# Kernel optimization log

Hardware: AMD Instinct MI355X
Metric: run time of the kernel (lower is better)

## Reference

```python
import jax, jax.numpy as jnp
import numpy as np

B, T, C = 8, 2048, 1024
DK = 64  # d_k = n_embd // n_head = 1024 // 16


def setup_inputs() -> dict:
    key = jax.random.key(0)
    ks = jax.random.split(key, 4)
    X = jax.random.normal(ks[0], (B, T, C), dtype=jnp.float32)
    scale = 1.0 / np.sqrt(C)
    Wq = jax.random.normal(ks[1], (C, DK), dtype=jnp.float32) * scale
    Wk = jax.random.normal(ks[2], (C, DK), dtype=jnp.float32) * scale
    Wv = jax.random.normal(ks[3], (C, DK), dtype=jnp.float32) * scale
    bq = jnp.zeros((DK,), dtype=jnp.float32)
    bk = jnp.zeros((DK,), dtype=jnp.float32)
    bv = jnp.zeros((DK,), dtype=jnp.float32)
    return {"X": X, "Wq": Wq, "bq": bq, "Wk": Wk, "bk": bk, "Wv": Wv, "bv": bv}


def reference(X, Wq, bq, Wk, bk, Wv, bv):
    # Single-head causal self-attention (dropout disabled / eval mode).
    T_ = X.shape[1]
    Q = X @ Wq + bq  # [B, T, d_k]
    K = X @ Wk + bk
    V = X @ Wv + bv
    scores = jnp.einsum('btd,bsd->bts', Q, K) / jnp.sqrt(jnp.float32(Q.shape[-1]))
    causal = jnp.tril(jnp.ones((T_, T_), dtype=bool))  # tril mask
    scores = jnp.where(causal, scores, -jnp.inf)
    weights = jax.nn.softmax(scores, axis=-1)
    out = jnp.einsum('bts,bsd->btd', weights, V)  # [B, T, d_k]
    return out
```

## Files before the change

### kernel.cpp

```cpp
#include <hip/hip_runtime.h>
#include <math.h>

#define NB 8
#define NT 2048
#define NC 1024
#define DK 64
#define BT (NB*NT)

#define QKV_BYTES  (3u * BT * DK * 2u)
#define SLOT_BYTES 8704u

typedef unsigned short ushort_t;
typedef unsigned int uint_t;
typedef __attribute__((ext_vector_type(8))) short short8;
typedef __attribute__((ext_vector_type(4))) float f32x4;

__device__ __forceinline__ float bf2f(uint_t u) {
    union { uint_t i; float f; } v;
    v.i = u << 16;
    return v.f;
}
__device__ __forceinline__ ushort_t f2bf(float f) {
    union { float f; uint_t i; } v; v.f = f;
    uint_t x = v.i;
    return (ushort_t)((x + 0x7fffu + ((x >> 16) & 1u)) >> 16);
}
__device__ __forceinline__ uint_t pack2bf(float lo, float hi) {
    return (uint_t)f2bf(lo) | ((uint_t)f2bf(hi) << 16);
}

__device__ __forceinline__ int seg_prefix(int qt) {
    const int a = qt >> 2;
    return 2 * a * (a + 1) - 4 + (qt & 3) * (a + 1);
}

__global__ __launch_bounds__(256) void wt_prep_kernel(
    const float* __restrict__ Wq, const float* __restrict__ Wk,
    const float* __restrict__ Wv, ushort_t* __restrict__ WtP)
{
    const int tid = blockIdx.x * 256 + threadIdx.x;
    int idx = tid;
    const int lane = idx & 63;  idx >>= 6;
    const int j    = idx % 6;   idx /= 6;
    const int w    = idx & 3;   idx >>= 2;
    const int ks   = idx & 7;   idx >>= 3;
    const int grp  = idx & 1;

    const int col = lane & 15;
    const int g   = lane >> 4;
    const int tj  = j >> 1;
    const int c   = j & 1;
    const int ng  = 48 * w + 16 * tj + col;
    const int which = ng >> 6, ncol = ng & 63;
    const float* W = (which == 0) ? Wq : (which == 1) ? Wk : Wv;
    const int kb = grp * 512 + ks * 64 + 32 * c + 8 * g;

    ushort_t o[8];
    #pragma unroll
    for (int i = 0; i < 8; ++i) o[i] = f2bf(W[(size_t)(kb + i) * DK + ncol]);
    *reinterpret_cast<uint4*>(&WtP[(size_t)tid * 8]) = *reinterpret_cast<uint4*>(o);
}

__global__ __launch_bounds__(512, 4) void qkv_mfma_kernel(
    const float* __restrict__ X, const ushort_t* __restrict__ WtP,
    const float* __restrict__ bq, const float* __restrict__ bk,
    const float* __restrict__ bv, ushort_t* __restrict__ QKV)
{
    __shared__ ushort_t Xs[2][2][32 * 72];
    __shared__ float    Racc[32 * 196];
    __shared__ ushort_t VtL[64 * 40];

    const int t    = threadIdx.x;
    const int grp  = t >> 8;
    const int tg   = t & 255;
    const int w    = (t >> 6) & 3;
    const int lane = t & 63;
    const int g    = lane >> 4;
    const int col  = lane & 15;
    const int m0   = blockIdx.x * 32;
    const int kb   = grp * 512;

    const int xrow = tg >> 3;
    const int xc   = (tg & 7) * 8;

    float xfA[8], xfB[8];
    short8 wA[6], wB[6];

    auto LOADX = [&](int k0, float* xf) {
        const float4* xp = reinterpret_cast<const float4*>(
            &X[(size_t)(m0 + xrow) * NC + kb + k0 + xc]);
        float4 v0 = xp[0], v1 = xp[1];
        xf[0] = v0.x; xf[1] = v0.y; xf[2] = v0.z; xf[3] = v0.w;
        xf[4] = v1.x; xf[5] = v1.y; xf[6] = v1.z; xf[7] = v1.w;
    };
    auto LOADW = [&](int ks, short8* wn) {
        const ushort_t* base = WtP + ((size_t)((grp * 8 + ks) * 4 + w)) * (6 * 64 * 8);
        #pragma unroll
        for (int j = 0; j < 6; ++j)
            wn[j] = *reinterpret_cast<const short8*>(base + (j * 64 + lane) * 8);
    };
    auto WRITEX = [&](int b, const float* xf) {
        ushort_t xb[8];
        #pragma unroll
        for (int j = 0; j < 8; ++j) xb[j] = f2bf(xf[j]);
        *reinterpret_cast<uint4*>(&Xs[grp][b][xrow * 72 + xc]) =
            *reinterpret_cast<uint4*>(xb);
    };

    f32x4 acc[2][3];
    #pragma unroll
    for (int ri = 0; ri < 2; ++ri)
        #pragma unroll
        for (int tj = 0; tj < 3; ++tj) acc[ri][tj] = (f32x4){0.f, 0.f, 0.f, 0.f};

    auto COMPUTE = [&](int cur, short8* wc) {
        const ushort_t* XsB = Xs[grp][cur];
        #pragma unroll
        for (int c = 0; c < 2; ++c) {
            short8 af[2];
            #pragma unroll
            for (int ri = 0; ri < 2; ++ri)
                af[ri] = *reinterpret_cast<const short8*>(
                    &XsB[(16 * ri + col) * 72 + 32 * c + 8 * g]);
            #pragma unroll
            for (int ri = 0; ri < 2; ++ri)
                #pragma unroll
                for (int tj = 0; tj < 3; ++tj)
                    acc[ri][tj] = __builtin_amdgcn_mfma_f32_16x16x32_bf16(
                        af[ri], wc[tj * 2 + c], acc[ri][tj], 0, 0, 0);
        }
    };

    LOADX(0, xfA);
    LOADW(0, wA);
    WRITEX(0, xfA);
    LOADX(64, xfB);

    #pragma unroll
    for (int ks2 = 0; ks2 < 4; ++ks2) {
        {
            const int ks = 2 * ks2;
            if (ks + 2 < 8) LOADX((ks + 2) * 64, xfA);
            if (ks < 7) LOADW(ks + 1, wB);
            __syncthreads();
            COMPUTE(0, wA);
            if (ks < 7) WRITEX(1, xfB);
        }
        {
            const int ks = 2 * ks2 + 1;
            if (ks + 2 < 8) LOADX((ks + 2) * 64, xfB);
            if (ks < 7) LOADW(ks + 1, wA);
            __syncthreads();
            COMPUTE(1, wB);
            if (ks < 7) WRITEX(0, xfA);
        }
    }

    __syncthreads();
    if (grp == 1) {
        #pragma unroll
        for (int ri = 0; ri < 2; ++ri)
            #pragma unroll
            for (int tj = 0; tj < 3; ++tj)
                #pragma unroll
                for (int r = 0; r < 4; ++r)
                    Racc[(16 * ri + 4 * g + r) * 196 + 48 * w + 16 * tj + col] =
                        acc[ri][tj][r];
    }
    __syncthreads();
    if (grp == 0) {
        #pragma unroll
        for (int ri = 0; ri < 2; ++ri)
            #pragma unroll
            for (int tj = 0; tj < 3; ++tj)
                #pragma unroll
                for (int r = 0; r < 4; ++r)
                    acc[ri][tj][r] +=
                        Racc[(16 * ri + 4 * g + r) * 196 + 48 * w + 16 * tj + col];
    }

    ushort_t* OutL = reinterpret_cast<ushort_t*>(Racc);

    if (grp == 0) {
        #pragma unroll
        for (int tj = 0; tj < 3; ++tj) {
            const int ng    = 48 * w + 16 * tj + col;
            const int which = ng >> 6, ncol = ng & 63;
            if (which == 2) {
                const float bb = bv[ncol];
                #pragma unroll
                for (int ri = 0; ri < 2; ++ri)
                    #pragma unroll
                    for (int r = 0; r < 4; ++r)
                        VtL[ncol * 40 + 16 * ri + 4 * g + r] = f2bf(acc[ri][tj][r] + bb);
            }
        }
    }

    #pragma unroll
    for (int pass = 0; pass < 2; ++pass) {
        __syncthreads();
        if (grp == 0) {
            #pragma unroll
            for (int tj = 0; tj < 3; ++tj) {
                const int ng    = 48 * w + 16 * tj + col;
                const int which = ng >> 6, ncol = ng & 63;
                if (which == pass) {
                    const float bb = (pass == 0) ? bq[ncol] : bk[ncol];
                    const float qs = (pass == 0) ? 0.125f : 1.0f;
                    #pragma unroll
                    for (int ri = 0; ri < 2; ++ri)
                        #pragma unroll
                        for (int r = 0; r < 4; ++r)
                            OutL[(16 * ri + 4 * g + r) * 72 + ncol] =
                                f2bf((acc[ri][tj][r] + bb) * qs);
                }
            }
        }
        __syncthreads();
        {
            ushort_t* Y = QKV + (size_t)pass * BT * DK;
            const int row = t >> 4;
            const int c4  = (t & 15) * 4;
            ushort4 v = *reinterpret_cast<const ushort4*>(&OutL[row * 72 + c4]);
            *reinterpret_cast<ushort4*>(&Y[(size_t)(m0 + row) * DK + c4]) = v;
        }
    }

    __syncthreads();
    {
        ushort_t* Vt = QKV + (size_t)2 * BT * DK;
        const int d  = t >> 3;
        const int sg = t & 7;
        ushort4 v = *reinterpret_cast<const ushort4*>(&VtL[d * 40 + sg * 4]);
        *reinterpret_cast<ushort4*>(&Vt[(size_t)d * BT + m0 + sg * 4]) = v;
    }
}

__global__ __launch_bounds__(256) void attn_seg_kernel(
    const ushort_t* __restrict__ QKV, float* __restrict__ Out,
    char* __restrict__ Pbase)
{
    const ushort_t* Qw = QKV;
    const ushort_t* Kw = QKV + (size_t)BT * DK;
    const ushort_t* Vw = QKV + (size_t)2 * BT * DK;

    __shared__ ushort_t Ks[256 * 72];
    __shared__ ushort_t VtL[64 * 288];

    const int t     = threadIdx.x;
    const int w     = t >> 6;
    const int lane  = t & 63;
    const int g     = lane >> 4;
    const int col   = lane & 15;
    const int batch = blockIdx.x & 7;
    const int u     = blockIdx.x >> 3;

    int s;
    if      (u < 16) s = 0;
    else if (u < 30) s = 1;
    else if (u < 42) s = 2;
    else if (u < 52) s = 3;
    else if (u < 60) s = 4;
    else if (u < 66) s = 5;
    else if (u < 70) s = 6;
    else             s = 7;
    const int off2 = 16 * s - s * (s - 1);
    const int qt0  = 4 * s + 2 * (u - off2);
    const int kbase = 256 * s;
    const int diag0 = qt0 - 4 * s;
    const int ntile = min(4, diag0 + 2);

    {
        const int sr = t >> 2;
        const int ss = t & 3;
        for (int i = 0; i < ntile; ++i) {
            const int krow = 64 * i + sr;
            const size_t gk = ((size_t)(batch * NT) + kbase + krow) * DK + ss * 16;
            const uint4* kp = reinterpret_cast<const uint4*>(Kw + gk);
            *reinterpret_cast<uint4*>(&Ks[krow * 72 + ss * 16])     = kp[0];
            *reinterpret_cast<uint4*>(&Ks[krow * 72 + ss * 16 + 8]) = kp[1];
            const size_t gv = (size_t)sr * BT + (batch * NT + kbase + 64 * i) + ss * 16;
            const uint4* vp = reinterpret_cast<const uint4*>(Vw + gv);
            *reinterpret_cast<uint4*>(&VtL[sr * 288 + 72 * i + ss * 16])     = vp[0];
            *reinterpret_cast<uint4*>(&VtL[sr * 288 + 72 * i + ss * 16 + 8]) = vp[1];
        }
    }
    __syncthreads();

    const int qrow0 = qt0 * 64 + 16 * w + col;
    const int qrow1 = qrow0 + 64;

    short8 q0a, q0b, q1a, q1b;
    {
        const ushort_t* Qr0 = Qw + ((size_t)(batch * NT) + qrow0) * DK;
        q0a = *reinterpret_cast<const short8*>(Qr0 + 8 * g);
        q0b = *reinterpret_cast<const short8*>(Qr0 + 32 + 8 * g);
        const ushort_t* Qr1 = Qw + ((size_t)(batch * NT) + qrow1) * DK;
        q1a = *reinterpret_cast<const short8*>(Qr1 + 8 * g);
        q1b = *reinterpret_cast<const short8*>(Qr1 + 32 + 8 * g);
    }

    f32x4 Oa0[4], Oa1[4];
    #pragma unroll
    for (int dt = 0; dt < 4; ++dt) {
        Oa0[dt] = (f32x4){0.f, 0.f, 0.f, 0.f};
        Oa1[dt] = (f32x4){0.f, 0.f, 0.f, 0.f};
    }
    float m0 = -INFINITY, l0 = 0.0f;
    float m1 = -INFINITY, l1 = 0.0f;

    for (int ktl = 0; ktl < ntile; ++ktl) {
        f32x4 sa0[4], sa1[4];
        #pragma unroll
        for (int tj = 0; tj < 4; ++tj) {
            sa0[tj] = (f32x4){0.f, 0.f, 0.f, 0.f};
            sa1[tj] = (f32x4){0.f, 0.f, 0.f, 0.f};
        }
        __builtin_amdgcn_s_setprio(1);
        #pragma unroll
        for (int tj = 0; tj < 4; ++tj) {
            const ushort_t* kb = &Ks[(64 * ktl + col + 16 * tj) * 72 + 8 * g];
            short8 kf0 = *reinterpret_cast<const short8*>(kb);
            short8 kf1 = *reinterpret_cast<const short8*>(kb + 32);
            sa0[tj] = __builtin_amdgcn_mfma_f32_16x16x32_bf16(kf0, q0a, sa0[tj], 0, 0, 0);
            sa0[tj] = __builtin_amdgcn_mfma_f32_16x16x32_bf16(kf1, q0b, sa0[tj], 0, 0, 0);
            sa1[tj] = __builtin_amdgcn_mfma_f32_16x16x32_bf16(kf0, q1a, sa1[tj], 0, 0, 0);
            sa1[tj] = __builtin_amdgcn_mfma_f32_16x16x32_bf16(kf1, q1b, sa1[tj], 0, 0, 0);
        }
        __builtin_amdgcn_s_setprio(0);

        const int s0 = kbase + 64 * ktl;
        if (ktl >= diag0) {
            #pragma unroll
            for (int tj = 0; tj < 4; ++tj)
                #pragma unroll
                for (int r = 0; r < 4; ++r)
                    if (s0 + 16 * tj + 4 * g + r > qrow0) sa0[tj][r] = -INFINITY;
        }
        if (ktl >= diag0 + 1) {
            #pragma unroll
            for (int tj = 0; tj < 4; ++tj)
                #pragma unroll
                for (int r = 0; r < 4; ++r)
                    if (s0 + 16 * tj + 4 * g + r > qrow1) sa1[tj][r] = -INFINITY;
        }

        float vx0 = sa0[0][0], vx1 = sa1[0][0];
        #pragma unroll
        for (int tj = 0; tj < 4; ++tj)
            #pragma unroll
            for (int r = 0; r < 4; ++r) {
                vx0 = fmaxf(vx0, sa0[tj][r]);
                vx1 = fmaxf(vx1, sa1[tj][r]);
            }
        vx0 = fmaxf(vx0, __shfl_xor(vx0, 16, 64));
        vx1 = fmaxf(vx1, __shfl_xor(vx1, 16, 64));
        vx0 = fmaxf(vx0, __shfl_xor(vx0, 32, 64));
        vx1 = fmaxf(vx1, __shfl_xor(vx1, 32, 64));

        const float mn0 = fmaxf(m0, vx0);
        const float mn1 = fmaxf(m1, vx1);
        const float sc0 = __expf(m0 - mn0);
        const float sc1 = __expf(m1 - mn1);
        m0 = mn0; m1 = mn1;

        float lt0 = 0.f, lt1 = 0.f;
        #pragma unroll
        for (int tj = 0; tj < 4; ++tj)
            #pragma unroll
            for (int r = 0; r < 4; ++r) {
                sa0[tj][r] = __expf(sa0[tj][r] - mn0);
                sa1[tj][r] = __expf(sa1[tj][r] - mn1);
                lt0 += sa0[tj][r];
                lt1 += sa1[tj][r];
            }
        lt0 += __shfl_xor(lt0, 16, 64);
        lt1 += __shfl_xor(lt1, 16, 64);
        lt0 += __shfl_xor(lt0, 32, 64);
        lt1 += __shfl_xor(lt1, 32, 64);
        l0 = l0 * sc0 + lt0;
        l1 = l1 * sc1 + lt1;

        float sco0[4], sco1[4];
        #pragma unroll
        for (int r = 0; r < 4; ++r) {
            sco0[r] = __shfl(sc0, 20 * g + r, 64);
            sco1[r] = __shfl(sc1, 20 * g + r, 64);
        }
        #pragma unroll
        for (int dt = 0; dt < 4; ++dt)
            #pragma unroll
            for (int r = 0; r < 4; ++r) {
                Oa0[dt][r] *= sco0[r];
                Oa1[dt][r] *= sco1[r];
            }

        uint_t pk00[4], pk01[4], pk10[4], pk11[4];
        #pragma unroll
        for (int tj = 0; tj < 4; ++tj) {
            pk00[tj] = pack2bf(sa0[tj][0], sa0[tj][1]);
            pk01[tj] = pack2bf(sa0[tj][2], sa0[tj][3]);
            pk10[tj] = pack2bf(sa1[tj][0], sa1[tj][1]);
            pk11[tj] = pack2bf(sa1[tj][2], sa1[tj][3]);
        }
        const int sA = col + 32 * (g & 1);
        const int sB = sA + 16;
        const bool hi = (g >= 2);

        #pragma unroll
        for (int c = 0; c < 2; ++c) {
            uint_t a0 = __shfl(pk00[2*c], sA, 64), b0 = __shfl(pk00[2*c+1], sA, 64);
            uint_t a1 = __shfl(pk01[2*c], sA, 64), b1 = __shfl(pk01[2*c+1], sA, 64);
            uint_t a2 = __shfl(pk00[2*c], sB, 64), b2 = __shfl(pk00[2*c+1], sB, 64);
            uint_t a3 = __shfl(pk01[2*c], sB, 64), b3 = __shfl(pk01[2*c+1], sB, 64);
            uint_t c0 = __shfl(pk10[2*c], sA, 64), d0 = __shfl(pk10[2*c+1], sA, 64);
            uint_t c1 = __shfl(pk11[2*c], sA, 64), d1 = __shfl(pk11[2*c+1], sA, 64);
            uint_t c2 = __shfl(pk10[2*c], sB, 64), d2 = __shfl(pk10[2*c+1], sB, 64);
            uint_t c3 = __shfl(pk11[2*c], sB, 64), d3 = __shfl(pk11[2*c+1], sB, 64);
            uint_t pa0[4], pa1[4];
            pa0[0] = hi ? b0 : a0;
            pa0[1] = hi ? b1 : a1;
            pa0[2] = hi ? b2 : a2;
            pa0[3] = hi ? b3 : a3;
            pa1[0] = hi ? d0 : c0;
            pa1[1] = hi ? d1 : c1;
            pa1[2] = hi ? d2 : c2;
            pa1[3] = hi ? d3 : c3;
            short8 paf0 = *reinterpret_cast<const short8*>(pa0);
            short8 paf1 = *reinterpret_cast<const short8*>(pa1);
            __builtin_amdgcn_s_setprio(1);
            #pragma unroll
            for (int dt = 0; dt < 4; ++dt) {
                short8 vf = *reinterpret_cast<const short8*>(
                    &VtL[(col + 16 * dt) * 288 + 72 * ktl + 32 * c + 8 * g]);
                Oa0[dt] = __builtin_amdgcn_mfma_f32_16x16x32_bf16(paf0, vf, Oa0[dt], 0, 0, 0);
                Oa1[dt] = __builtin_amdgcn_mfma_f32_16x16x32_bf16(paf1, vf, Oa1[dt], 0, 0, 0);
            }
            __builtin_amdgcn_s_setprio(0);
        }
    }

    #pragma unroll
    for (int iq = 0; iq < 2; ++iq) {
        const int qt = qt0 + iq;
        const float mm = iq ? m1 : m0;
        const float ll = iq ? l1 : l0;
        const f32x4* Oa = iq ? Oa1 : Oa0;

        float lr[4];
        #pragma unroll
        for (int r = 0; r < 4; ++r) lr[r] = __shfl(ll, 20 * g + r, 64);

        if (qt < 4) {
            #pragma unroll
            for (int r = 0; r < 4; ++r) {
                const float inv = 1.0f / lr[r];
                const int row = qt * 64 + 16 * w + 4 * g + r;
                float* op = Out + ((size_t)(batch * NT) + row) * DK + col;
                #pragma unroll
                for (int dt = 0; dt < 4; ++dt) op[16 * dt] = Oa[dt][r] * inv;
            }
        } else {
            float mr[4];
            #pragma unroll
            for (int r = 0; r < 4; ++r) mr[r] = __shfl(mm, 20 * g + r, 64);
            const int slot = batch * 140 + seg_prefix(qt) + s;
            char* sp = Pbase + (size_t)slot * SLOT_BYTES;
            ushort_t* Ob  = reinterpret_cast<ushort_t*>(sp);
            float*    Pm  = reinterpret_cast<float*>(sp + 8192);
            float*    Plv = reinterpret_cast<float*>(sp + 8448);
            #pragma unroll
            for (int r = 0; r < 4; ++r) {
                const int rloc = 16 * w + 4 * g + r;
                #pragma unroll
                for (int dt = 0; dt < 4; ++dt)
                    Ob[rloc * 64 + 16 * dt + col] = f2bf(Oa[dt][r]);
                if (col == 0) { Pm[rloc] = mr[r]; Plv[rloc] = lr[r]; }
            }
        }
    }
}

__global__ __launch_bounds__(256) void attn_combine_kernel(
    const char* __restrict__ Pbase, float* __restrict__ Out)
{
    const int bid   = blockIdx.x;
    const int batch = bid / 28;
    const int qt    = 4 + bid % 28;
    const int nseg  = (qt >> 2) + 1;
    const int slot0 = batch * 140 + seg_prefix(qt);

    const int t   = threadIdx.x;
    const int row = t >> 2;
    const int d0  = (t & 3) * 16;

    float ms[8], ls[8];
    float M = -INFINITY;
    #pragma unroll
    for (int s = 0; s < 8; ++s)
        if (s < nseg) {
            const char* sp = Pbase + (size_t)(slot0 + s) * SLOT_BYTES;
            ms[s] = reinterpret_cast<const float*>(sp + 8192)[row];
            ls[s] = reinterpret_cast<const float*>(sp + 8448)[row];
            M = fmaxf(M, ms[s]);
        }

    float acc[16];
    #pragma unroll
    for (int j = 0; j < 16; ++j) acc[j] = 0.f;
    float ltot = 0.f;

    #pragma unroll
    for (int s = 0; s < 8; ++s)
        if (s < nseg) {
            const float wsc = __expf(ms[s] - M);
            ltot += wsc * ls[s];
            const ushort_t* Ob = reinterpret_cast<const ushort_t*>(
                Pbase + (size_t)(slot0 + s) * SLOT_BYTES) + row * 64 + d0;
            uint4 u0 = *reinterpret_cast<const uint4*>(Ob);
            uint4 u1 = *reinterpret_cast<const uint4*>(Ob + 8);
            const uint_t* uu = reinterpret_cast<const uint_t*>(&u0);
            #pragma unroll
            for (int j = 0; j < 4; ++j) {
                acc[2*j+0] += wsc * bf2f(uu[j] & 0xffffu);
                acc[2*j+1] += wsc * bf2f(uu[j] >> 16);
            }
            const uint_t* uv = reinterpret_cast<const uint_t*>(&u1);
            #pragma unroll
            for (int j = 0; j < 4; ++j) {
                acc[8+2*j+0] += wsc * bf2f(uv[j] & 0xffffu);
                acc[8+2*j+1] += wsc * bf2f(uv[j] >> 16);
            }
        }

    const float inv = 1.0f / ltot;
    float* op = Out + ((size_t)(batch * NT) + qt * 64 + row) * DK + d0;
    #pragma unroll
    for (int j = 0; j < 16; ++j) op[j] = acc[j] * inv;
}

extern "C" void kernel_launch(void* const* d_in, const int* in_sizes, int n_in,
                              void* d_out, int out_size, void* d_ws, size_t ws_size,
                              hipStream_t stream) {
    const float* X  = (const float*)d_in[0];
    const float* Wq = (const float*)d_in[1];
    const float* bq = (const float*)d_in[2];
    const float* Wk = (const float*)d_in[3];
    const float* bk = (const float*)d_in[4];
    const float* Wv = (const float*)d_in[5];
    const float* bv = (const float*)d_in[6];
    float* Out = (float*)d_out;
    ushort_t* QKV = (ushort_t*)d_ws;
    char* Pbase   = (char*)d_ws + QKV_BYTES;
    ushort_t* WtP = (ushort_t*)d_out;

    wt_prep_kernel<<<96, 256, 0, stream>>>(Wq, Wk, Wv, WtP);
    qkv_mfma_kernel<<<512, 512, 0, stream>>>(X, WtP, bq, bk, bv, QKV);
    attn_seg_kernel<<<576, 256, 0, stream>>>(QKV, Out, Pbase);
    attn_combine_kernel<<<224, 256, 0, stream>>>(Pbase, Out);
}
```

Baseline: 55.47 us.

## Load X fragments directly from global into MFMA registers, dropping LDS staging

The QKV projection kernel no longer stages X tiles through double-buffered shared memory with barriers. Each lane now reads its own MFMA A-fragment straight from global memory, converts it to bf16 and feeds the MFMA. This removes the LDS writes, LDS reads and per-step __syncthreads. In exchange, the four waves of each group redundantly load the same X rows, and the explicit software prefetch pipeline is gone, so load latency is left to the compiler's unrolled scheduling.

```diff
diff --git a/kernel.cpp b/kernel.cpp
--- a/kernel.cpp
+++ b/kernel.cpp
@@ -66,13 +66,11 @@
     const float* __restrict__ bq, const float* __restrict__ bk,
     const float* __restrict__ bv, ushort_t* __restrict__ QKV)
 {
-    __shared__ ushort_t Xs[2][2][32 * 72];
     __shared__ float    Racc[32 * 196];
     __shared__ ushort_t VtL[64 * 40];
 
     const int t    = threadIdx.x;
     const int grp  = t >> 8;
-    const int tg   = t & 255;
     const int w    = (t >> 6) & 3;
     const int lane = t & 63;
     const int g    = lane >> 4;
@@ -80,32 +78,10 @@
     const int m0   = blockIdx.x * 32;
     const int kb   = grp * 512;
 
-    const int xrow = tg >> 3;
-    const int xc   = (tg & 7) * 8;
-
-    float xfA[8], xfB[8];
-    short8 wA[6], wB[6];
-
-    auto LOADX = [&](int k0, float* xf) {
-        const float4* xp = reinterpret_cast<const float4*>(
-            &X[(size_t)(m0 + xrow) * NC + kb + k0 + xc]);
-        float4 v0 = xp[0], v1 = xp[1];
-        xf[0] = v0.x; xf[1] = v0.y; xf[2] = v0.z; xf[3] = v0.w;
-        xf[4] = v1.x; xf[5] = v1.y; xf[6] = v1.z; xf[7] = v1.w;
-    };
-    auto LOADW = [&](int ks, short8* wn) {
-        const ushort_t* base = WtP + ((size_t)((grp * 8 + ks) * 4 + w)) * (6 * 64 * 8);
-        #pragma unroll
-        for (int j = 0; j < 6; ++j)
-            wn[j] = *reinterpret_cast<const short8*>(base + (j * 64 + lane) * 8);
-    };
-    auto WRITEX = [&](int b, const float* xf) {
-        ushort_t xb[8];
-        #pragma unroll
-        for (int j = 0; j < 8; ++j) xb[j] = f2bf(xf[j]);
-        *reinterpret_cast<uint4*>(&Xs[grp][b][xrow * 72 + xc]) =
-            *reinterpret_cast<uint4*>(xb);
-    };
+    const float* xp00 = X + (size_t)(m0 + col) * NC      + kb + 8 * g;
+    const float* xp01 = xp00 + 32;
+    const float* xp10 = X + (size_t)(m0 + 16 + col) * NC + kb + 8 * g;
+    const float* xp11 = xp10 + 32;
 
     f32x4 acc[2][3];
     #pragma unroll
@@ -113,47 +89,37 @@
         #pragma unroll
         for (int tj = 0; tj < 3; ++tj) acc[ri][tj] = (f32x4){0.f, 0.f, 0.f, 0.f};
 
-    auto COMPUTE = [&](int cur, short8* wc) {
-        const ushort_t* XsB = Xs[grp][cur];
-        #pragma unroll
-        for (int c = 0; c < 2; ++c) {
-            short8 af[2];
-            #pragma unroll
-            for (int ri = 0; ri < 2; ++ri)
-                af[ri] = *reinterpret_cast<const short8*>(
-                    &XsB[(16 * ri + col) * 72 + 32 * c + 8 * g]);
+    #pragma unroll
+    for (int ks = 0; ks < 8; ++ks) {
+        short8 af[2][2];
+        {
+            const float* ps[4] = { xp00 + ks * 64, xp01 + ks * 64,
+                                   xp10 + ks * 64, xp11 + ks * 64 };
+            #pragma unroll
+            for (int q = 0; q < 4; ++q) {
+                float4 v0 = reinterpret_cast<const float4*>(ps[q])[0];
+                float4 v1 = reinterpret_cast<const float4*>(ps[q])[1];
+                ushort_t b[8];
+                b[0] = f2bf(v0.x); b[1] = f2bf(v0.y); b[2] = f2bf(v0.z); b[3] = f2bf(v0.w);
+                b[4] = f2bf(v1.x); b[5] = f2bf(v1.y); b[6] = f2bf(v1.z); b[7] = f2bf(v1.w);
+                af[q >> 1][q & 1] = *reinterpret_cast<const short8*>(b);
+            }
+        }
+        short8 wf[6];
+        {
+            const ushort_t* base = WtP + ((size_t)((grp * 8 + ks) * 4 + w)) * (6 * 64 * 8);
+            #pragma unroll
+            for (int j = 0; j < 6; ++j)
+                wf[j] = *reinterpret_cast<const short8*>(base + (j * 64 + lane) * 8);
+        }
+        #pragma unroll
+        for (int c = 0; c < 2; ++c)
             #pragma unroll
             for (int ri = 0; ri < 2; ++ri)
                 #pragma unroll
                 for (int tj = 0; tj < 3; ++tj)
                     acc[ri][tj] = __builtin_amdgcn_mfma_f32_16x16x32_bf16(
-                        af[ri], wc[tj * 2 + c], acc[ri][tj], 0, 0, 0);
-        }
-    };
-
-    LOADX(0, xfA);
-    LOADW(0, wA);
-    WRITEX(0, xfA);
-    LOADX(64, xfB);
-
-    #pragma unroll
-    for (int ks2 = 0; ks2 < 4; ++ks2) {
-        {
-            const int ks = 2 * ks2;
-            if (ks + 2 < 8) LOADX((ks + 2) * 64, xfA);
-            if (ks < 7) LOADW(ks + 1, wB);
-            __syncthreads();
-            COMPUTE(0, wA);
-            if (ks < 7) WRITEX(1, xfB);
-        }
-        {
-            const int ks = 2 * ks2 + 1;
-            if (ks + 2 < 8) LOADX((ks + 2) * 64, xfB);
-            if (ks < 7) LOADW(ks + 1, wA);
-            __syncthreads();
-            COMPUTE(1, wB);
-            if (ks < 7) WRITEX(0, xfA);
-        }
+                        af[ri][c], wf[tj * 2 + c], acc[ri][tj], 0, 0, 0);
     }
 
     __syncthreads();
```

After: 76.58 us. 1.38x slower.

## Double QKV projection row tile to 64 and overlay shared buffers via union

Applied to the files above, without the earlier changes.

The QKV projection kernel now gives each block 64 rows instead of 32. Each block reuses the weight fragments it loads from global memory across twice as many MFMA tiles, which halves total weight traffic, and the grid shrinks to 256 blocks. Shared memory is overlaid in a union so the larger X tiles and the reduction/output buffers fit, and output stores are widened to 16-byte vectors. The X prefetch pipeline depth drops from two stages to one, and with 256 blocks on a 256-CU part, occupancy and latency hiding may suffer.

```diff
diff --git a/kernel.cpp b/kernel.cpp
--- a/kernel.cpp
+++ b/kernel.cpp
@@ -61,14 +61,16 @@
     *reinterpret_cast<uint4*>(&WtP[(size_t)tid * 8]) = *reinterpret_cast<uint4*>(o);
 }
 
-__global__ __launch_bounds__(512, 4) void qkv_mfma_kernel(
+__global__ __launch_bounds__(512) void qkv_mfma_kernel(
     const float* __restrict__ X, const ushort_t* __restrict__ WtP,
     const float* __restrict__ bq, const float* __restrict__ bk,
     const float* __restrict__ bv, ushort_t* __restrict__ QKV)
 {
-    __shared__ ushort_t Xs[2][2][32 * 72];
-    __shared__ float    Racc[32 * 196];
-    __shared__ ushort_t VtL[64 * 40];
+    union SMemU {
+        ushort_t xs[2][2][64 * 72];
+        struct { float racc[64 * 196]; ushort_t vtl[64 * 72]; } e;
+    };
+    __shared__ SMemU sm;
 
     const int t    = threadIdx.x;
     const int grp  = t >> 8;
@@ -77,21 +79,23 @@
     const int lane = t & 63;
     const int g    = lane >> 4;
     const int col  = lane & 15;
-    const int m0   = blockIdx.x * 32;
+    const int m0   = blockIdx.x * 64;
     const int kb   = grp * 512;
 
-    const int xrow = tg >> 3;
-    const int xc   = (tg & 7) * 8;
-
-    float xfA[8], xfB[8];
+    const int xrow = tg >> 2;
+    const int xc   = (tg & 3) * 16;
+
+    float xf[16];
     short8 wA[6], wB[6];
 
-    auto LOADX = [&](int k0, float* xf) {
+    auto LOADX = [&](int k0) {
         const float4* xp = reinterpret_cast<const float4*>(
             &X[(size_t)(m0 + xrow) * NC + kb + k0 + xc]);
-        float4 v0 = xp[0], v1 = xp[1];
-        xf[0] = v0.x; xf[1] = v0.y; xf[2] = v0.z; xf[3] = v0.w;
-        xf[4] = v1.x; xf[5] = v1.y; xf[6] = v1.z; xf[7] = v1.w;
+        #pragma unroll
+        for (int j = 0; j < 4; ++j) {
+            float4 v = xp[j];
+            xf[4*j+0] = v.x; xf[4*j+1] = v.y; xf[4*j+2] = v.z; xf[4*j+3] = v.w;
+        }
     };
     auto LOADW = [&](int ks, short8* wn) {
         const ushort_t* base = WtP + ((size_t)((grp * 8 + ks) * 4 + w)) * (6 * 64 * 8);
@@ -99,31 +103,33 @@
         for (int j = 0; j < 6; ++j)
             wn[j] = *reinterpret_cast<const short8*>(base + (j * 64 + lane) * 8);
     };
-    auto WRITEX = [&](int b, const float* xf) {
-        ushort_t xb[8];
-        #pragma unroll
-        for (int j = 0; j < 8; ++j) xb[j] = f2bf(xf[j]);
-        *reinterpret_cast<uint4*>(&Xs[grp][b][xrow * 72 + xc]) =
-            *reinterpret_cast<uint4*>(xb);
+    auto WRITEX = [&](int b) {
+        ushort_t xb[16];
+        #pragma unroll
+        for (int j = 0; j < 16; ++j) xb[j] = f2bf(xf[j]);
+        *reinterpret_cast<uint4*>(&sm.xs[grp][b][xrow * 72 + xc])     =
+            reinterpret_cast<uint4*>(xb)[0];
+        *reinterpret_cast<uint4*>(&sm.xs[grp][b][xrow * 72 + xc + 8]) =
+            reinterpret_cast<uint4*>(xb)[1];
     };
 
-    f32x4 acc[2][3];
-    #pragma unroll
-    for (int ri = 0; ri < 2; ++ri)
+    f32x4 acc[4][3];
+    #pragma unroll
+    for (int ri = 0; ri < 4; ++ri)
         #pragma unroll
         for (int tj = 0; tj < 3; ++tj) acc[ri][tj] = (f32x4){0.f, 0.f, 0.f, 0.f};
 
     auto COMPUTE = [&](int cur, short8* wc) {
-        const ushort_t* XsB = Xs[grp][cur];
+        const ushort_t* XsB = sm.xs[grp][cur];
         #pragma unroll
         for (int c = 0; c < 2; ++c) {
-            short8 af[2];
-            #pragma unroll
-            for (int ri = 0; ri < 2; ++ri)
+            short8 af[4];
+            #pragma unroll
+            for (int ri = 0; ri < 4; ++ri)
                 af[ri] = *reinterpret_cast<const short8*>(
                     &XsB[(16 * ri + col) * 72 + 32 * c + 8 * g]);
             #pragma unroll
-            for (int ri = 0; ri < 2; ++ri)
+            for (int ri = 0; ri < 4; ++ri)
                 #pragma unroll
                 for (int tj = 0; tj < 3; ++tj)
                     acc[ri][tj] = __builtin_amdgcn_mfma_f32_16x16x32_bf16(
@@ -131,57 +137,50 @@
         }
     };
 
-    LOADX(0, xfA);
+    LOADX(0);
     LOADW(0, wA);
-    WRITEX(0, xfA);
-    LOADX(64, xfB);
+    WRITEX(0);
 
     #pragma unroll
     for (int ks2 = 0; ks2 < 4; ++ks2) {
         {
             const int ks = 2 * ks2;
-            if (ks + 2 < 8) LOADX((ks + 2) * 64, xfA);
-            if (ks < 7) LOADW(ks + 1, wB);
+            if (ks < 7) { LOADX((ks + 1) * 64); LOADW(ks + 1, wB); }
             __syncthreads();
             COMPUTE(0, wA);
-            if (ks < 7) WRITEX(1, xfB);
+            if (ks < 7) WRITEX(1);
         }
         {
             const int ks = 2 * ks2 + 1;
-            if (ks + 2 < 8) LOADX((ks + 2) * 64, xfB);
-            if (ks < 7) LOADW(ks + 1, wA);
+            if (ks < 7) { LOADX((ks + 1) * 64); LOADW(ks + 1, wA); }
             __syncthreads();
             COMPUTE(1, wB);
-            if (ks < 7) WRITEX(0, xfA);
+            if (ks < 7) WRITEX(0);
         }
     }
 
     __syncthreads();
     if (grp == 1) {
         #pragma unroll
-        for (int ri = 0; ri < 2; ++ri)
+        for (int ri = 0; ri < 4; ++ri)
             #pragma unroll
             for (int tj = 0; tj < 3; ++tj)
                 #pragma unroll
                 for (int r = 0; r < 4; ++r)
-                    Racc[(16 * ri + 4 * g + r) * 196 + 48 * w + 16 * tj + col] =
+                    sm.e.racc[(16 * ri + 4 * g + r) * 196 + 48 * w + 16 * tj + col] =
                         acc[ri][tj][r];
     }
     __syncthreads();
     if (grp == 0) {
         #pragma unroll
-        for (int ri = 0; ri < 2; ++ri)
+        for (int ri = 0; ri < 4; ++ri)
             #pragma unroll
             for (int tj = 0; tj < 3; ++tj)
                 #pragma unroll
                 for (int r = 0; r < 4; ++r)
                     acc[ri][tj][r] +=
-                        Racc[(16 * ri + 4 * g + r) * 196 + 48 * w + 16 * tj + col];
-    }
-
-    ushort_t* OutL = reinterpret_cast<ushort_t*>(Racc);
-
-    if (grp == 0) {
+                        sm.e.racc[(16 * ri + 4 * g + r) * 196 + 48 * w + 16 * tj + col];
+
         #pragma unroll
         for (int tj = 0; tj < 3; ++tj) {
             const int ng    = 48 * w + 16 * tj + col;
@@ -189,13 +188,16 @@
             if (which == 2) {
                 const float bb = bv[ncol];
                 #pragma unroll
-                for (int ri = 0; ri < 2; ++ri)
+                for (int ri = 0; ri < 4; ++ri)
                     #pragma unroll
                     for (int r = 0; r < 4; ++r)
-                        VtL[ncol * 40 + 16 * ri + 4 * g + r] = f2bf(acc[ri][tj][r] + bb);
-            }
-        }
-    }
+                        sm.e.vtl[ncol * 72 + 16 * ri + 4 * g + r] =
+                            f2bf(acc[ri][tj][r] + bb);
+            }
+        }
+    }
+
+    ushort_t* OutL = reinterpret_cast<ushort_t*>(sm.e.racc);
 
     #pragma unroll
     for (int pass = 0; pass < 2; ++pass) {
@@ -209,7 +211,7 @@
                     const float bb = (pass == 0) ? bq[ncol] : bk[ncol];
                     const float qs = (pass == 0) ? 0.125f : 1.0f;
                     #pragma unroll
-                    for (int ri = 0; ri < 2; ++ri)
+                    for (int ri = 0; ri < 4; ++ri)
                         #pragma unroll
                         for (int r = 0; r < 4; ++r)
                             OutL[(16 * ri + 4 * g + r) * 72 + ncol] =
@@ -220,10 +222,10 @@
         __syncthreads();
         {
             ushort_t* Y = QKV + (size_t)pass * BT * DK;
-            const int row = t >> 4;
-            const int c4  = (t & 15) * 4;
-            ushort4 v = *reinterpret_cast<const ushort4*>(&OutL[row * 72 + c4]);
-            *reinterpret_cast<ushort4*>(&Y[(size_t)(m0 + row) * DK + c4]) = v;
+            const int row = t >> 3;
+            const int c8  = (t & 7) * 8;
+            uint4 v = *reinterpret_cast<const uint4*>(&OutL[row * 72 + c8]);
+            *reinterpret_cast<uint4*>(&Y[(size_t)(m0 + row) * DK + c8]) = v;
         }
     }
 
@@ -232,8 +234,8 @@
         ushort_t* Vt = QKV + (size_t)2 * BT * DK;
         const int d  = t >> 3;
         const int sg = t & 7;
-        ushort4 v = *reinterpret_cast<const ushort4*>(&VtL[d * 40 + sg * 4]);
-        *reinterpret_cast<ushort4*>(&Vt[(size_t)d * BT + m0 + sg * 4]) = v;
+        uint4 v = *reinterpret_cast<const uint4*>(&sm.e.vtl[d * 72 + sg * 8]);
+        *reinterpret_cast<uint4*>(&Vt[(size_t)d * BT + m0 + sg * 8]) = v;
     }
 }
 
@@ -556,7 +558,7 @@
     ushort_t* WtP = (ushort_t*)d_out;
 
     wt_prep_kernel<<<96, 256, 0, stream>>>(Wq, Wk, Wv, WtP);
-    qkv_mfma_kernel<<<512, 512, 0, stream>>>(X, WtP, bq, bk, bv, QKV);
+    qkv_mfma_kernel<<<256, 512, 0, stream>>>(X, WtP, bq, bk, bv, QKV);
     attn_seg_kernel<<<576, 256, 0, stream>>>(QKV, Out, Pbase);
     attn_combine_kernel<<<224, 256, 0, stream>>>(Pbase, Out);
 }
```

New measurement: 54.27 us, median of 2. 2.2% less time.
